# Kernel optimization log

Measured on AMD Instinct MI355X. Metric: run time of the kernel, lower is better.

Reference implementation:

```python
import jax, jax.numpy as jnp
import numpy as np

K = 5            # spline kernel size per dim
NUM_CLASSES = 10
EPS = 1e-4       # matches module's normalize eps
ROUTING_ITERS = 3
_BITS = jnp.array([[(b >> 2) & 1, (b >> 1) & 1, b & 1] for b in range(8)], dtype=jnp.float32)  # [8,3]


def normalize(t, axis=-1):
    return t / (jnp.sqrt(jnp.sum(t * t, axis=axis, keepdims=True)) + EPS)


def quat_mul(q, r):
    # quaternions stored (x, y, z, w) -- module sets identity as [:,:,:,3]=1
    qx, qy, qz, qw = q[..., 0], q[..., 1], q[..., 2], q[..., 3]
    rx, ry, rz, rw = r[..., 0], r[..., 1], r[..., 2], r[..., 3]
    return jnp.stack([
        qw * rx + qx * rw + qy * rz - qz * ry,
        qw * ry - qx * rz + qy * rw + qz * rx,
        qw * rz + qx * ry - qy * rx + qz * rw,
        qw * rw - qx * rx - qy * ry - qz * rz,
    ], axis=-1)


def spline_conv(x, pseudo, src, dst, W, root, bias, n_nodes):
    # degree-1 open B-spline conv, kernel 5^3, in=1, out=16
    v = pseudo * (K - 1)                                   # [E,3]
    i0 = jnp.clip(jnp.floor(v), 0, K - 2)                  # [E,3]
    frac = v - i0
    i0 = i0.astype(jnp.int32)
    idx = i0[:, None, :] + _BITS.astype(jnp.int32)[None]   # [E,8,3]
    kflat = (idx[..., 0] * K + idx[..., 1]) * K + idx[..., 2]  # [E,8]
    wb = jnp.prod(jnp.where(_BITS[None] > 0, frac[:, None, :], 1.0 - frac[:, None, :]), axis=-1)  # [E,8]
    Wg = W[kflat]                                          # [E,8,16] irregular gather (dominant traffic)
    wk = jnp.einsum('eb,ebo->eo', wb, Wg)                  # [E,16]
    msg = x[src] * wk                                      # [E,16] (in-channels = 1)
    agg = jax.ops.segment_sum(msg, dst, num_segments=n_nodes)
    deg = jax.ops.segment_sum(jnp.ones_like(dst, dtype=x.dtype), dst, num_segments=n_nodes)
    return agg / jnp.maximum(deg, 1.0)[:, None] + x @ root + bias


def caps_layer(pose, act, q):
    # pose [N,I,4], act [N,I], q [I,J,4] -> pose [N,J,4], act [N,J]
    qn = normalize(q)
    pred = normalize(quat_mul(qn[None], pose[:, :, None, :]))  # [N,I,J,4]
    b = jnp.zeros(pred.shape[:3], dtype=pose.dtype)
    for _ in range(ROUTING_ITERS):
        c = jax.nn.softmax(b, axis=2) * act[:, :, None]
        s = jnp.einsum('nij,nijq->njq', c, pred)
        v = normalize(s)
        b = b + jnp.einsum('nijq,njq->nij', pred, v)
    act_out = jax.nn.sigmoid(jnp.einsum('nij,nijq,njq->nj', c, pred, v))
    return v, act_out


def pool_by_agreement(pose, act, pos, G, start, size):
    # voxel-grid clustering + agreement-weighted quaternion averaging
    g = jnp.clip(jnp.floor((pos - start) / size), 0, G - 1).astype(jnp.int32)  # [N,3]
    vid = (g[:, 0] * G + g[:, 1]) * G + g[:, 2]
    V = G ** 3
    s = jax.ops.segment_sum(act[:, :, None] * pose, vid, num_segments=V)  # [V,J,4]
    m = normalize(s)
    agree = jnp.sum(pose * m[vid], axis=-1)                                # [N,J]
    wsum = jax.ops.segment_sum(act, vid, num_segments=V)
    cnt = jax.ops.segment_sum(jnp.ones((pose.shape[0],), pose.dtype), vid, num_segments=V)
    act_out = jax.nn.sigmoid(jax.ops.segment_sum(act * agree, vid, num_segments=V) / (wsum + EPS))
    pos_out = jax.ops.segment_sum(pos, vid, num_segments=V) / (cnt[:, None] + EPS)
    return m, act_out, pos_out


def forward(x, pos, pseudo, W_spline, root, bias, lin_w, lin_b, q0, q1, q3, q5, q6, q7, edge_index):
    N = x.shape[0]
    src, dst = edge_index[0], edge_index[1]
    h = spline_conv(x, pseudo, src, dst, W_spline, root, bias, N)   # [N,16]
    quats = jax.nn.elu(h) @ lin_w + lin_b                           # [N,4]
    pose = normalize(quats.reshape(N, 1, 4))                        # [N,1,4]
    act = x.reshape(N, 1)                                           # expand to num_caps_in=1
    pose, act = caps_layer(pose, act, q0)                           # 1 -> 6
    pose, act = caps_layer(pose, act, q1)                           # 6 -> 6
    min_pos, max_pos = pos.min(), pos.max()
    rng = max_pos + 0.001 - min_pos
    pose, act, p = pool_by_agreement(pose, act, pos, 32, min_pos, rng / 32)   # -> 32768 voxels
    pose, act = caps_layer(pose, act, q3)                           # 6 -> 8
    pose, act, p = pool_by_agreement(pose, act, p, 8, min_pos, rng / 8)       # -> 512
    pose, act = caps_layer(pose, act, q5)                           # 8 -> 12
    pose, act, p = pool_by_agreement(pose, act, p, 2, min_pos, rng / 2)       # -> 8
    pose, act = caps_layer(pose, act, q6)                           # 12 -> 14
    pose, act, p = pool_by_agreement(pose, act, p, 1, min_pos - 0.5, max_pos - min_pos + 1.0)  # -> 1
    pose, act = caps_layer(pose, act, q7)                           # 14 -> 10
    return act                                                      # [1, 10]


def setup_inputs() -> dict:
    key = jax.random.key(0)
    ks = jax.random.split(key, 16)
    N, E = 50000, 800000
    def caps_q(k, i, j):
        return jax.random.normal(k, (i, j, 4), dtype=jnp.float32)
    return {
        'x': jax.random.uniform(ks[0], (N, 1), dtype=jnp.float32),
        'pos': jax.random.uniform(ks[1], (N, 3), dtype=jnp.float32),
        'pseudo': jax.random.uniform(ks[2], (E, 3), dtype=jnp.float32),
        'W_spline': jax.random.normal(ks[3], (K ** 3, 16), dtype=jnp.float32) * 0.1,
        'root': jax.random.normal(ks[4], (1, 16), dtype=jnp.float32) * 0.1,
        'bias': jnp.zeros((16,), dtype=jnp.float32),
        'lin_w': jax.random.normal(ks[5], (16, 4), dtype=jnp.float32) * 0.25,
        'lin_b': jnp.zeros((4,), dtype=jnp.float32),
        'q0': caps_q(ks[6], 1, 6),
        'q1': caps_q(ks[7], 6, 6),
        'q3': caps_q(ks[8], 6, 8),
        'q5': caps_q(ks[9], 8, 12),
        'q6': caps_q(ks[10], 12, 14),
        'q7': caps_q(ks[11], 14, NUM_CLASSES),
        'edge_index': jax.random.randint(ks[12], (2, E), 0, N, dtype=jnp.int32),
    }


def reference(x, pos, pseudo, W_spline, root, bias, lin_w, lin_b, q0, q1, q3, q5, q6, q7, edge_index):
    return forward(x, pos, pseudo, W_spline, root, bias, lin_w, lin_b, q0, q1, q3, q5, q6, q7, edge_index)
```

## Files before the change

kernel.cpp:

```cpp
#include <hip/hip_runtime.h>
#include <math.h>

#define EPS 1e-4f

__device__ __forceinline__ float sigmoidf_(float x){ return 1.0f/(1.0f+expf(-x)); }

__device__ __forceinline__ unsigned f2u_(float f){
    unsigned u = __float_as_uint(f);
    return (u & 0x80000000u) ? ~u : (u | 0x80000000u);
}
__device__ __forceinline__ float u2f_(unsigned u){
    unsigned b = (u & 0x80000000u) ? (u & 0x7FFFFFFFu) : ~u;
    return __uint_as_float(b);
}

__global__ void minmax_kernel(const float* __restrict__ p, int n, unsigned* mm){
    float lo = INFINITY, hi = -INFINITY;
    for (int i = blockIdx.x*blockDim.x + threadIdx.x; i < n; i += gridDim.x*blockDim.x){
        float v = p[i]; lo = fminf(lo, v); hi = fmaxf(hi, v);
    }
    for (int off = 32; off > 0; off >>= 1){
        lo = fminf(lo, __shfl_down(lo, off));
        hi = fmaxf(hi, __shfl_down(hi, off));
    }
    __shared__ float slo[8], shi[8];
    int wid = threadIdx.x >> 6;
    if ((threadIdx.x & 63) == 0){ slo[wid] = lo; shi[wid] = hi; }
    __syncthreads();
    if (threadIdx.x == 0){
        int nw = blockDim.x >> 6;
        for (int w = 1; w < nw; w++){ lo = fminf(lo, slo[w]); hi = fmaxf(hi, shi[w]); }
        atomicMin(&mm[0], f2u_(lo));
        atomicMax(&mm[1], f2u_(hi));
    }
}


__global__ void edge_rank(const int* __restrict__ ei, int* __restrict__ deg,
                          int* __restrict__ rank, int E){
    int e = blockIdx.x*blockDim.x + threadIdx.x;
    if (e >= E) return;
    rank[e] = atomicAdd(&deg[ei[E + e]], 1);
}

__global__ __launch_bounds__(256)
void scan_bsum(const int* __restrict__ deg, int* __restrict__ bsum, int N){
    int i = blockIdx.x*256 + threadIdx.x;
    int v = (i < N) ? deg[i] : 0;
    for (int o = 32; o > 0; o >>= 1) v += __shfl_down(v, o);
    __shared__ int ws[4];
    if ((threadIdx.x & 63) == 0) ws[threadIdx.x >> 6] = v;
    __syncthreads();
    if (threadIdx.x == 0) bsum[blockIdx.x] = ws[0] + ws[1] + ws[2] + ws[3];
}

__global__ __launch_bounds__(1024)
void scan_top(int* __restrict__ bsum, int NB){
    __shared__ int sh[1024];
    int t = threadIdx.x;
    int v = (t < NB) ? bsum[t] : 0;
    sh[t] = v;
    __syncthreads();
    for (int d = 1; d < 1024; d <<= 1){
        int u = (t >= d) ? sh[t - d] : 0;
        __syncthreads();
        sh[t] += u;
        __syncthreads();
    }
    if (t < NB) bsum[t] = sh[t] - v;
    if (t == 1023) bsum[NB] = sh[1023];
}

__global__ __launch_bounds__(256)
void scan_final(const int* __restrict__ deg, const int* __restrict__ bsum,
                int* __restrict__ off, int N, int NB){
    __shared__ int sh[256];
    int b = blockIdx.x;
    int i = b*256 + threadIdx.x;
    int v = (i < N) ? deg[i] : 0;
    sh[threadIdx.x] = v;
    __syncthreads();
    for (int d = 1; d < 256; d <<= 1){
        int u = (threadIdx.x >= d) ? sh[threadIdx.x - d] : 0;
        __syncthreads();
        sh[threadIdx.x] += u;
        __syncthreads();
    }
    if (i < N) off[i] = bsum[b] + sh[threadIdx.x] - v;
    if (b == 0 && threadIdx.x == 0) off[N] = bsum[NB];
}

__global__ void edge_pack(const int* __restrict__ ei, const float* __restrict__ pseudo,
                          const float* __restrict__ x,
                          const int* __restrict__ rank, const int* __restrict__ off,
                          float4* __restrict__ rec4, int* __restrict__ recb, int E){
    int e = blockIdx.x*blockDim.x + threadIdx.x;
    if (e >= E) return;
    float p0 = pseudo[3*e], p1 = pseudo[3*e+1], p2 = pseudo[3*e+2];
    int s = ei[e], d = ei[E + e];
    float v0 = p0*4.f, v1 = p1*4.f, v2 = p2*4.f;
    float f0 = fminf(fmaxf(floorf(v0), 0.f), 3.f);
    float f1 = fminf(fmaxf(floorf(v1), 0.f), 3.f);
    float f2 = fminf(fmaxf(floorf(v2), 0.f), 3.f);
    int slot = off[d] + rank[e];
    rec4[slot] = make_float4(v0 - f0, v1 - f1, v2 - f2, x[s]);
    recb[slot] = ((int)f0*5 + (int)f1)*5 + (int)f2;
}

__device__ __forceinline__ int voxel_id(const float* __restrict__ pos, int n, int G,
                                        float start, float size){
    int g[3];
    #pragma unroll
    for (int k = 0; k < 3; k++){
        float gg = floorf((pos[(size_t)n*3 + k] - start) / size);
        gg = fminf(fmaxf(gg, 0.f), (float)(G - 1));
        g[k] = (int)gg;
    }
    return (g[0]*G + g[1])*G + g[2];
}

__device__ __forceinline__ void pool_geom(const unsigned* mm, int G, int mode,
                                          float& start, float& size){
    float mn = u2f_(mm[0]), mx = u2f_(mm[1]);
    if (mode == 0){ start = mn; size = (mx + 0.001f - mn) / (float)G; }
    else          { start = mn - 0.5f; size = mx - mn + 1.0f; }
}

__global__ void elist_node(const float* __restrict__ pos, int* __restrict__ head,
                           int* __restrict__ nxt, int N, int G, int mode,
                           const unsigned* __restrict__ mm){
    int n = blockIdx.x*blockDim.x + threadIdx.x;
    if (n >= N) return;
    float start, size; pool_geom(mm, G, mode, start, size);
    int v = voxel_id(pos, n, G, start, size);
    nxt[n] = atomicExch(&head[v], n);
}

__global__ __launch_bounds__(256)
void spline_node_kernel(const float* __restrict__ x, const float4* __restrict__ rec4,
                        const int* __restrict__ recb, const int* __restrict__ off,
                        const float* __restrict__ W,
                        const float* __restrict__ root, const float* __restrict__ bias,
                        const float* __restrict__ lin_w, const float* __restrict__ lin_b,
                        float* __restrict__ pose, float* __restrict__ act, int N){
    __shared__ float Ws[125*17];
    for (int i = threadIdx.x; i < 125*16; i += blockDim.x)
        Ws[(i >> 4)*17 + (i & 15)] = W[i];
    __syncthreads();
    int t = blockIdx.x*blockDim.x + threadIdx.x;
    int n = t >> 3;
    int k = t & 7;
    if (n >= N) return;

    int o0 = off[n], o1 = off[n+1];

    float agg[16];
    #pragma unroll
    for (int o = 0; o < 16; o++) agg[o] = 0.f;

    for (int s = o0 + k; s < o1; s += 8){
        float4 rv = rec4[s];
        int base = recb[s];
        float fr0 = rv.x, fr1 = rv.y, fr2 = rv.z, xv = rv.w;
        #pragma unroll
        for (int b = 0; b < 8; b++){
            int b0 = (b >> 2) & 1, b1 = (b >> 1) & 1, b2 = b & 1;
            float w = (b0 ? fr0 : 1.f - fr0) * (b1 ? fr1 : 1.f - fr1) * (b2 ? fr2 : 1.f - fr2);
            w *= xv;
            const float* Wr = &Ws[(base + b0*25 + b1*5 + b2)*17];
            #pragma unroll
            for (int o = 0; o < 16; o++) agg[o] += w * Wr[o];
        }
    }

    #pragma unroll
    for (int o = 0; o < 16; o++){
        agg[o] += __shfl_xor(agg[o], 1);
        agg[o] += __shfl_xor(agg[o], 2);
        agg[o] += __shfl_xor(agg[o], 4);
    }

    if (k != 0) return;

    float deg = fmaxf((float)(o1 - o0), 1.0f);
    float xs = x[n];
    float qv0 = lin_b[0], qv1 = lin_b[1], qv2 = lin_b[2], qv3 = lin_b[3];
    #pragma unroll
    for (int o = 0; o < 16; o++){
        float h = agg[o] / deg + xs * root[o] + bias[o];
        float e = (h > 0.f) ? h : expm1f(h);
        qv0 += e * lin_w[o*4 + 0];
        qv1 += e * lin_w[o*4 + 1];
        qv2 += e * lin_w[o*4 + 2];
        qv3 += e * lin_w[o*4 + 3];
    }
    float inv = 1.0f / (sqrtf(qv0*qv0 + qv1*qv1 + qv2*qv2 + qv3*qv3) + EPS);
    pose[(size_t)n*4 + 0] = qv0*inv;
    pose[(size_t)n*4 + 1] = qv1*inv;
    pose[(size_t)n*4 + 2] = qv2*inv;
    pose[(size_t)n*4 + 3] = qv3*inv;
    act[n] = xs;
}

template<int I, int J, int NPB>
__global__ __launch_bounds__(NPB*I*J)
void caps_coop_kernel(const float* __restrict__ poseIn, const float* __restrict__ actIn,
                      const float* __restrict__ q, float* __restrict__ poseOut,
                      float* __restrict__ actOut, int N){
    const int IJ = I*J;
    const int tid = threadIdx.x;
    const int nl  = tid / IJ;
    const int li  = tid - nl*IJ;
    const int i   = li / J;
    const int j   = li - i*J;
    const int node = blockIdx.x*NPB + nl;
    const bool on = (node < N);

    __shared__ float redA[NPB][I*J];
    __shared__ float redB[NPB][I*J];
    __shared__ float cp[NPB][I*J*4];
    __shared__ float vsh[NPB][J*4];

    float prx=0.f, pry=0.f, prz=0.f, prw=0.f, ai=0.f;
    if (on){
        float qx = q[li*4+0], qy = q[li*4+1], qz = q[li*4+2], qw = q[li*4+3];
        float qinv = 1.0f/(sqrtf(qx*qx+qy*qy+qz*qz+qw*qw)+EPS);
        qx*=qinv; qy*=qinv; qz*=qinv; qw*=qinv;
        const float* pp = &poseIn[((size_t)node*I + i)*4];
        float rx=pp[0], ry=pp[1], rz=pp[2], rw=pp[3];
        ai = actIn[(size_t)node*I + i];
        float tx = qw*rx + qx*rw + qy*rz - qz*ry;
        float ty = qw*ry - qx*rz + qy*rw + qz*rx;
        float tz = qw*rz + qx*ry - qy*rx + qz*rw;
        float tw = qw*rw - qx*rx - qy*ry - qz*rz;
        float pinv = 1.0f/(sqrtf(tx*tx+ty*ty+tz*tz+tw*tw)+EPS);
        prx=tx*pinv; pry=ty*pinv; prz=tz*pinv; prw=tw*pinv;
    }

    float b = 0.f, c = 0.f;
    for (int t = 0; t < 3; t++){
        redA[nl][li] = b;
        __syncthreads();
        float mb = -INFINITY;
        #pragma unroll
        for (int jj = 0; jj < J; jj++) mb = fmaxf(mb, redA[nl][i*J+jj]);
        float e = expf(b - mb);
        redB[nl][li] = e;
        __syncthreads();
        float s = 0.f;
        #pragma unroll
        for (int jj = 0; jj < J; jj++) s += redB[nl][i*J+jj];
        c = ai * e / s;
        cp[nl][li*4+0] = c*prx; cp[nl][li*4+1] = c*pry;
        cp[nl][li*4+2] = c*prz; cp[nl][li*4+3] = c*prw;
        __syncthreads();
        for (int idx = li; idx < J*4; idx += IJ){
            int jj = idx >> 2, comp = idx & 3;
            float acc = 0.f;
            #pragma unroll
            for (int ii = 0; ii < I; ii++) acc += cp[nl][(ii*J+jj)*4+comp];
            vsh[nl][idx] = acc;
        }
        __syncthreads();
        if (li < J){
            float a0=vsh[nl][li*4], a1=vsh[nl][li*4+1], a2=vsh[nl][li*4+2], a3=vsh[nl][li*4+3];
            float inv = 1.0f/(sqrtf(a0*a0+a1*a1+a2*a2+a3*a3)+EPS);
            vsh[nl][li*4]=a0*inv; vsh[nl][li*4+1]=a1*inv;
            vsh[nl][li*4+2]=a2*inv; vsh[nl][li*4+3]=a3*inv;
        }
        __syncthreads();
        if (t < 2){
            b += prx*vsh[nl][j*4] + pry*vsh[nl][j*4+1] + prz*vsh[nl][j*4+2] + prw*vsh[nl][j*4+3];
            __syncthreads();
        } else {
            redA[nl][li] = c*(prx*vsh[nl][j*4] + pry*vsh[nl][j*4+1]
                            + prz*vsh[nl][j*4+2] + prw*vsh[nl][j*4+3]);
            __syncthreads();
            if (li < J && on){
                float acc = 0.f;
                #pragma unroll
                for (int ii = 0; ii < I; ii++) acc += redA[nl][ii*J+li];
                actOut[(size_t)node*J + li] = sigmoidf_(acc);
                poseOut[((size_t)node*J+li)*4+0] = vsh[nl][li*4+0];
                poseOut[((size_t)node*J+li)*4+1] = vsh[nl][li*4+1];
                poseOut[((size_t)node*J+li)*4+2] = vsh[nl][li*4+2];
                poseOut[((size_t)node*J+li)*4+3] = vsh[nl][li*4+3];
            }
        }
    }
}

template<int J>
__global__ __launch_bounds__(256)
void pool1_gather_kernel(const float* __restrict__ pose, const float* __restrict__ act,
                         const float* __restrict__ pos,
                         const int* __restrict__ head, const int* __restrict__ nxt,
                         float* __restrict__ poseOut, float* __restrict__ actOut,
                         float* __restrict__ posOut, int V){
    int v = blockIdx.x*blockDim.x + threadIdx.x;
    if (v >= V) return;

    float s[J][4], w[J], ps0=0.f, ps1=0.f, ps2=0.f;
    #pragma unroll
    for (int j = 0; j < J; j++){ s[j][0]=0.f; s[j][1]=0.f; s[j][2]=0.f; s[j][3]=0.f; w[j]=0.f; }

    int cnt = 0;
    for (int n = head[v]; n >= 0; n = nxt[n]){
        const float* pb = &pose[(size_t)n*J*4];
        const float* ab = &act[(size_t)n*J];
        #pragma unroll
        for (int j = 0; j < J; j++){
            float aj = ab[j];
            s[j][0] += aj*pb[j*4+0];
            s[j][1] += aj*pb[j*4+1];
            s[j][2] += aj*pb[j*4+2];
            s[j][3] += aj*pb[j*4+3];
            w[j] += aj;
        }
        ps0 += pos[(size_t)n*3+0];
        ps1 += pos[(size_t)n*3+1];
        ps2 += pos[(size_t)n*3+2];
        cnt++;
    }
    #pragma unroll
    for (int j = 0; j < J; j++){
        float inv = 1.0f/(sqrtf(s[j][0]*s[j][0]+s[j][1]*s[j][1]+
                                s[j][2]*s[j][2]+s[j][3]*s[j][3])+EPS);
        s[j][0]*=inv; s[j][1]*=inv; s[j][2]*=inv; s[j][3]*=inv;
    }
    float ag[J];
    #pragma unroll
    for (int j = 0; j < J; j++) ag[j] = 0.f;
    for (int n = head[v]; n >= 0; n = nxt[n]){
        const float* pb = &pose[(size_t)n*J*4];
        const float* ab = &act[(size_t)n*J];
        #pragma unroll
        for (int j = 0; j < J; j++){
            float agree = pb[j*4+0]*s[j][0] + pb[j*4+1]*s[j][1]
                        + pb[j*4+2]*s[j][2] + pb[j*4+3]*s[j][3];
            ag[j] += ab[j]*agree;
        }
    }
    #pragma unroll
    for (int j = 0; j < J; j++){
        size_t o = (size_t)v*J + j;
        actOut[o] = sigmoidf_(ag[j] / (w[j] + EPS));
        poseOut[o*4+0] = s[j][0];
        poseOut[o*4+1] = s[j][1];
        poseOut[o*4+2] = s[j][2];
        poseOut[o*4+3] = s[j][3];
    }
    float c = (float)cnt + EPS;
    posOut[(size_t)v*3+0] = ps0 / c;
    posOut[(size_t)v*3+1] = ps1 / c;
    posOut[(size_t)v*3+2] = ps2 / c;
}

template<int V, int J, int CH, int NCHUNK>
__global__ void pool_priv1(const float4* __restrict__ poseIn, const float* __restrict__ actIn,
                           const float* __restrict__ posIn,
                           float* __restrict__ s, float* __restrict__ wsum,
                           float* __restrict__ cnt, float* __restrict__ psum,
                           int N, int G, int mode, const unsigned* __restrict__ mm){
    __shared__ float s_[V*CH*4];
    __shared__ float wsum_[V*CH];
    __shared__ float cnt_[V];
    __shared__ float psum_[V*3];
    const int chunk = blockIdx.x % NCHUNK;
    const int slice = blockIdx.x / NCHUNK;
    const int nslices = gridDim.x / NCHUNK;
    const int c0 = chunk * CH;

    for (int t = threadIdx.x; t < V*CH*4; t += blockDim.x) s_[t] = 0.f;
    for (int t = threadIdx.x; t < V*CH; t += blockDim.x) wsum_[t] = 0.f;
    if (chunk == 0){
        for (int t = threadIdx.x; t < V; t += blockDim.x) cnt_[t] = 0.f;
        for (int t = threadIdx.x; t < V*3; t += blockDim.x) psum_[t] = 0.f;
    }
    __syncthreads();

    float start, size; pool_geom(mm, G, mode, start, size);
    int per = (N + nslices - 1) / nslices;
    int n0 = slice * per, n1 = min(N, n0 + per);

    for (int n = n0 + (int)threadIdx.x; n < n1; n += blockDim.x){
        int vid = voxel_id(posIn, n, G, start, size);
        #pragma unroll
        for (int jj = 0; jj < CH; jj++){
            int j = c0 + jj;
            float aj = actIn[(size_t)n*J + j];
            float4 p = poseIn[(size_t)n*J + j];
            int b = (vid*CH + jj)*4;
            atomicAdd(&s_[b+0], aj*p.x);
            atomicAdd(&s_[b+1], aj*p.y);
            atomicAdd(&s_[b+2], aj*p.z);
            atomicAdd(&s_[b+3], aj*p.w);
            atomicAdd(&wsum_[vid*CH + jj], aj);
        }
        if (chunk == 0){
            atomicAdd(&cnt_[vid], 1.0f);
            atomicAdd(&psum_[vid*3+0], posIn[(size_t)n*3+0]);
            atomicAdd(&psum_[vid*3+1], posIn[(size_t)n*3+1]);
            atomicAdd(&psum_[vid*3+2], posIn[(size_t)n*3+2]);
        }
    }
    __syncthreads();

    for (int t = threadIdx.x; t < V*CH*4; t += blockDim.x){
        float val = s_[t];
        if (val != 0.f){
            int v = t / (CH*4), r = t % (CH*4);
            atomicAdd(&s[((size_t)v*J + c0)*4 + r], val);
        }
    }
    for (int t = threadIdx.x; t < V*CH; t += blockDim.x){
        float val = wsum_[t];
        if (val != 0.f){
            int v = t / CH, jj = t % CH;
            atomicAdd(&wsum[(size_t)v*J + c0 + jj], val);
        }
    }
    if (chunk == 0){
        for (int t = threadIdx.x; t < V; t += blockDim.x)
            if (cnt_[t] != 0.f) atomicAdd(&cnt[t], cnt_[t]);
        for (int t = threadIdx.x; t < V*3; t += blockDim.x)
            if (psum_[t] != 0.f) atomicAdd(&psum[t], psum_[t]);
    }
}

template<int V, int J>
__global__ void pool_priv2(const float4* __restrict__ poseIn, const float* __restrict__ actIn,
                           const float* __restrict__ posIn, const float4* __restrict__ m,
                           float* __restrict__ agacc,
                           int N, int G, int mode, const unsigned* __restrict__ mm){
    __shared__ float ag_[V*J];
    for (int t = threadIdx.x; t < V*J; t += blockDim.x) ag_[t] = 0.f;
    __syncthreads();
    float start, size; pool_geom(mm, G, mode, start, size);
    int nslices = gridDim.x;
    int per = (N + nslices - 1) / nslices;
    int n0 = blockIdx.x * per, n1 = min(N, n0 + per);
    for (int n = n0 + (int)threadIdx.x; n < n1; n += blockDim.x){
        int vid = voxel_id(posIn, n, G, start, size);
        #pragma unroll
        for (int j = 0; j < J; j++){
            float4 p  = poseIn[(size_t)n*J + j];
            float4 mv = m[(size_t)vid*J + j];
            float agree = p.x*mv.x + p.y*mv.y + p.z*mv.z + p.w*mv.w;
            atomicAdd(&ag_[vid*J + j], actIn[(size_t)n*J + j]*agree);
        }
    }
    __syncthreads();
    for (int t = threadIdx.x; t < V*J; t += blockDim.x)
        if (ag_[t] != 0.f) atomicAdd(&agacc[t], ag_[t]);
}

__global__ void pool_m(const float* __restrict__ s, float* __restrict__ m, int VJ){
    int t = blockIdx.x*blockDim.x + threadIdx.x;
    if (t >= VJ) return;
    float a = s[(size_t)t*4], b = s[(size_t)t*4+1], c = s[(size_t)t*4+2], d = s[(size_t)t*4+3];
    float inv = 1.0f / (sqrtf(a*a + b*b + c*c + d*d) + EPS);
    m[(size_t)t*4]   = a*inv;
    m[(size_t)t*4+1] = b*inv;
    m[(size_t)t*4+2] = c*inv;
    m[(size_t)t*4+3] = d*inv;
}

__global__ void pool_fin(const float* __restrict__ agacc, const float* __restrict__ wsum,
                         const float* __restrict__ cnt, const float* __restrict__ psum,
                         float* __restrict__ actOut, float* __restrict__ posOut, int V, int J){
    int t = blockIdx.x*blockDim.x + threadIdx.x;
    if (t >= V*J) return;
    int v = t / J, j = t % J;
    actOut[t] = sigmoidf_(agacc[t] / (wsum[t] + EPS));
    if (j == 0){
        float c = cnt[v] + EPS;
        posOut[(size_t)v*3 + 0] = psum[(size_t)v*3 + 0] / c;
        posOut[(size_t)v*3 + 1] = psum[(size_t)v*3 + 1] / c;
        posOut[(size_t)v*3 + 2] = psum[(size_t)v*3 + 2] / c;
    }
}

template<int V, int J, int CH>
__global__ void pool_fused_kernel(const float* __restrict__ poseIn, const float* __restrict__ actIn,
                                  const float* __restrict__ posIn,
                                  float* __restrict__ poseOut, float* __restrict__ actOut,
                                  float* __restrict__ posOut,
                                  int N, int G, int mode, const unsigned* __restrict__ mm){
    __shared__ float s_[V*CH*4];
    __shared__ float wsum_[V*CH];
    __shared__ float ag_[V*CH];
    __shared__ float cnt_[V];
    __shared__ float psum_[V*3];
    const int c0 = blockIdx.x * CH;

    for (int t = threadIdx.x; t < V*CH*4; t += blockDim.x) s_[t] = 0.f;
    for (int t = threadIdx.x; t < V*CH; t += blockDim.x){ wsum_[t] = 0.f; ag_[t] = 0.f; }
    if (blockIdx.x == 0){
        for (int t = threadIdx.x; t < V; t += blockDim.x) cnt_[t] = 0.f;
        for (int t = threadIdx.x; t < V*3; t += blockDim.x) psum_[t] = 0.f;
    }
    __syncthreads();

    float start, size; pool_geom(mm, G, mode, start, size);

    for (int n = threadIdx.x; n < N; n += blockDim.x){
        int vid = voxel_id(posIn, n, G, start, size);
        #pragma unroll
        for (int jj = 0; jj < CH; jj++){
            int j = c0 + jj;
            float aj = actIn[(size_t)n*J + j];
            const float* pb = &poseIn[((size_t)n*J + j)*4];
            int b = (vid*CH + jj)*4;
            atomicAdd(&s_[b+0], aj*pb[0]);
            atomicAdd(&s_[b+1], aj*pb[1]);
            atomicAdd(&s_[b+2], aj*pb[2]);
            atomicAdd(&s_[b+3], aj*pb[3]);
            atomicAdd(&wsum_[vid*CH + jj], aj);
        }
        if (blockIdx.x == 0){
            atomicAdd(&cnt_[vid], 1.0f);
            atomicAdd(&psum_[vid*3+0], posIn[(size_t)n*3+0]);
            atomicAdd(&psum_[vid*3+1], posIn[(size_t)n*3+1]);
            atomicAdd(&psum_[vid*3+2], posIn[(size_t)n*3+2]);
        }
    }
    __syncthreads();

    for (int t = threadIdx.x; t < V*CH; t += blockDim.x){
        float a = s_[t*4], b = s_[t*4+1], c = s_[t*4+2], d = s_[t*4+3];
        float inv = 1.0f / (sqrtf(a*a + b*b + c*c + d*d) + EPS);
        s_[t*4] = a*inv; s_[t*4+1] = b*inv; s_[t*4+2] = c*inv; s_[t*4+3] = d*inv;
    }
    __syncthreads();

    for (int n = threadIdx.x; n < N; n += blockDim.x){
        int vid = voxel_id(posIn, n, G, start, size);
        #pragma unroll
        for (int jj = 0; jj < CH; jj++){
            int j = c0 + jj;
            const float* pb = &poseIn[((size_t)n*J + j)*4];
            const float* mb = &s_[(vid*CH + jj)*4];
            float agree = pb[0]*mb[0] + pb[1]*mb[1] + pb[2]*mb[2] + pb[3]*mb[3];
            atomicAdd(&ag_[vid*CH + jj], actIn[(size_t)n*J + j]*agree);
        }
    }
    __syncthreads();

    for (int t = threadIdx.x; t < V*CH; t += blockDim.x){
        int v = t / CH, jj = t % CH;
        size_t o = (size_t)v*J + c0 + jj;
        actOut[o] = sigmoidf_(ag_[t] / (wsum_[t] + EPS));
        poseOut[o*4+0] = s_[t*4+0];
        poseOut[o*4+1] = s_[t*4+1];
        poseOut[o*4+2] = s_[t*4+2];
        poseOut[o*4+3] = s_[t*4+3];
    }
    if (blockIdx.x == 0){
        for (int v = threadIdx.x; v < V; v += blockDim.x){
            float c = cnt_[v] + EPS;
            posOut[(size_t)v*3+0] = psum_[(size_t)v*3+0] / c;
            posOut[(size_t)v*3+1] = psum_[(size_t)v*3+1] / c;
            posOut[(size_t)v*3+2] = psum_[(size_t)v*3+2] / c;
        }
    }
}

extern "C" void kernel_launch(void* const* d_in, const int* in_sizes, int n_in,
                              void* d_out, int out_size, void* d_ws, size_t ws_size,
                              hipStream_t stream){
    const float* x      = (const float*)d_in[0];
    const float* pos    = (const float*)d_in[1];
    const float* pseudo = (const float*)d_in[2];
    const float* Wsp    = (const float*)d_in[3];
    const float* root   = (const float*)d_in[4];
    const float* bias   = (const float*)d_in[5];
    const float* lin_w  = (const float*)d_in[6];
    const float* lin_b  = (const float*)d_in[7];
    const float* q0     = (const float*)d_in[8];
    const float* q1     = (const float*)d_in[9];
    const float* q3     = (const float*)d_in[10];
    const float* q5     = (const float*)d_in[11];
    const float* q6     = (const float*)d_in[12];
    const float* q7     = (const float*)d_in[13];
    const int*   ei     = (const int*)d_in[14];
    const int N = in_sizes[0];
    const int E = in_sizes[2] / 3;
    const int V1 = 32768;
    const int NB = (N + 255)/256;

    char* ws = (char*)d_ws;
    size_t off = 0;
    auto alloc = [&](size_t bytes)->void*{
        void* p = ws + off;
        off += (bytes + 255) & ~(size_t)255;
        return p;
    };
    unsigned* mm   = (unsigned*)alloc(8);
    int* deg       = (int*)alloc((size_t)N*sizeof(int));
    int* erank     = (int*)alloc((size_t)E*sizeof(int));
    int* eoff      = (int*)alloc((size_t)(N+1)*sizeof(int));
    int* bsum      = (int*)alloc((size_t)(NB+1)*sizeof(int));
    float4* rec4   = (float4*)alloc((size_t)E*sizeof(float4));
    int* recb      = (int*)alloc((size_t)E*sizeof(int));
    int* vhead     = (int*)alloc((size_t)V1*sizeof(int));
    int* vnxt      = (int*)alloc((size_t)N*sizeof(int));
    float* P0  = (float*)alloc((size_t)1250000*sizeof(float));
    float* P1  = (float*)alloc((size_t)1250000*sizeof(float));
    float* A0  = (float*)alloc((size_t)310000*sizeof(float));
    float* A1  = (float*)alloc((size_t)310000*sizeof(float));
    float* PB0 = (float*)alloc((size_t)100000*sizeof(float));
    float* PB1 = (float*)alloc((size_t)100000*sizeof(float));
    size_t pool_off0 = off;
    float* vs  = (float*)alloc((size_t)512*8*4*sizeof(float));
    float* vw  = (float*)alloc((size_t)512*8*sizeof(float));
    float* va  = (float*)alloc((size_t)512*8*sizeof(float));
    float* vc  = (float*)alloc((size_t)512*sizeof(float));
    float* vp  = (float*)alloc((size_t)512*3*sizeof(float));
    size_t pool_bytes = off - pool_off0;

    hipMemsetAsync(mm,     0xFF, 4, stream);
    hipMemsetAsync(mm + 1, 0x00, 4, stream);
    hipMemsetAsync(deg, 0, (size_t)N*sizeof(int), stream);
    hipMemsetAsync(vhead, 0xFF, (size_t)V1*sizeof(int), stream);

    minmax_kernel<<<80, 256, 0, stream>>>(pos, N*3, mm);

    edge_rank<<<(E + 255)/256, 256, 0, stream>>>(ei, deg, erank, E);
    scan_bsum<<<NB, 256, 0, stream>>>(deg, bsum, N);
    scan_top<<<1, 1024, 0, stream>>>(bsum, NB);
    scan_final<<<NB, 256, 0, stream>>>(deg, bsum, eoff, N, NB);
    edge_pack<<<(E + 255)/256, 256, 0, stream>>>(ei, pseudo, x, erank, eoff, rec4, recb, E);
    spline_node_kernel<<<(8*N + 255)/256, 256, 0, stream>>>(x, rec4, recb, eoff, Wsp,
                                                            root, bias, lin_w, lin_b, P0, A0, N);

    caps_coop_kernel<1,6,32><<<(N + 31)/32, 32*6, 0, stream>>>(P0, A0, q0, P1, A1, N);
    caps_coop_kernel<6,6,7><<<(N + 6)/7, 7*36, 0, stream>>>(P1, A1, q1, P0, A0, N);

    {
        const int G = 32;
        elist_node<<<(N + 255)/256, 256, 0, stream>>>(pos, vhead, vnxt, N, G, 0, mm);
        pool1_gather_kernel<6><<<(V1 + 255)/256, 256, 0, stream>>>(P0, A0, pos, vhead, vnxt,
                                                                   P1, A1, PB0, V1);
    }
    caps_coop_kernel<6,8,5><<<(32768 + 4)/5, 5*48, 0, stream>>>(P1, A1, q3, P0, A0, 32768);

    {
        const int V = 512, J = 8, G = 8, NSL = 64;
        hipMemsetAsync(vs, 0, pool_bytes, stream);
        pool_priv1<V,J,4,2><<<2*NSL, 256, 0, stream>>>((const float4*)P0, A0, PB0,
                                                       vs, vw, vc, vp, 32768, G, 0, mm);
        pool_m<<<(V*J + 255)/256, 256, 0, stream>>>(vs, P1, V*J);
        pool_priv2<V,J><<<NSL, 256, 0, stream>>>((const float4*)P0, A0, PB0,
                                                 (const float4*)P1, va, 32768, G, 0, mm);
        pool_fin<<<(V*J + 255)/256, 256, 0, stream>>>(va, vw, vc, vp, A1, PB1, V, J);
    }
    caps_coop_kernel<8,12,2><<<256, 2*96, 0, stream>>>(P1, A1, q5, P0, A0, 512);

    {
        const int V = 8, J = 12, G = 2, NSL = 16;
        hipMemsetAsync(vs, 0, pool_bytes, stream);
        pool_priv1<V,J,12,1><<<NSL, 256, 0, stream>>>((const float4*)P0, A0, PB1,
                                                      vs, vw, vc, vp, 512, G, 0, mm);
        pool_m<<<1, 256, 0, stream>>>(vs, P1, V*J);
        pool_priv2<V,J><<<NSL, 256, 0, stream>>>((const float4*)P0, A0, PB1,
                                                 (const float4*)P1, va, 512, G, 0, mm);
        pool_fin<<<1, 256, 0, stream>>>(va, vw, vc, vp, A1, PB0, V, J);
    }
    caps_coop_kernel<12,14,1><<<8, 168, 0, stream>>>(P1, A1, q6, P0, A0, 8);

    pool_fused_kernel<1,14,14><<<1, 1024, 0, stream>>>(P0, A0, PB0, P1, A1, PB1, 8, 1, 1, mm);
    caps_coop_kernel<14,10,1><<<1, 140, 0, stream>>>(P1, A1, q7, P0, (float*)d_out, 1);
}
```

Measured before the change: 349.5 us.

## Use thread-per-node capsule routing for early layers and fuse small pooling stage

Adds a capsule routing kernel that gives each node to a single thread. That thread holds all predictions and routing logits in registers, which replaces the cooperative block kernel that used shared-memory reductions for the three large early capsule layers. The small second pooling stage, a memset plus four kernel launches, is also replaced by one call to the existing fused pooling kernel. The aim is to remove shared-memory reduction and synchronisation overhead and launch count. The cost is heavy register pressure for the 6x8 layer, which may spill or lower occupancy.

```diff
diff --git a/kernel.cpp b/kernel.cpp
--- a/kernel.cpp
+++ b/kernel.cpp
@@ -34,7 +34,6 @@
         atomicMax(&mm[1], f2u_(hi));
     }
 }
-
 
 __global__ void edge_rank(const int* __restrict__ ei, int* __restrict__ deg,
                           int* __restrict__ rank, int E){
@@ -200,6 +199,90 @@
     pose[(size_t)n*4 + 2] = qv2*inv;
     pose[(size_t)n*4 + 3] = qv3*inv;
     act[n] = xs;
+}
+
+template<int I, int J>
+__global__ __launch_bounds__(64)
+void caps_node_kernel(const float* __restrict__ poseIn, const float* __restrict__ actIn,
+                      const float* __restrict__ q,
+                      float* __restrict__ poseOut, float* __restrict__ actOut, int N){
+    __shared__ float qn[I*J*4];
+    for (int t = threadIdx.x; t < I*J; t += blockDim.x){
+        float qa=q[t*4], qb=q[t*4+1], qc=q[t*4+2], qd=q[t*4+3];
+        float inv = 1.f/(sqrtf(qa*qa+qb*qb+qc*qc+qd*qd)+EPS);
+        qn[t*4+0]=qa*inv; qn[t*4+1]=qb*inv; qn[t*4+2]=qc*inv; qn[t*4+3]=qd*inv;
+    }
+    __syncthreads();
+    int n = blockIdx.x*blockDim.x + threadIdx.x;
+    if (n >= N) return;
+
+    float pr[I][J][4];
+    float a[I];
+    float b[I][J];
+    #pragma unroll
+    for (int i = 0; i < I; i++){
+        float4 p = *reinterpret_cast<const float4*>(&poseIn[((size_t)n*I + i)*4]);
+        a[i] = actIn[(size_t)n*I + i];
+        #pragma unroll
+        for (int j = 0; j < J; j++){
+            const float* qq = &qn[(i*J + j)*4];
+            float qx=qq[0], qy=qq[1], qz=qq[2], qw=qq[3];
+            float tx = qw*p.x + qx*p.w + qy*p.z - qz*p.y;
+            float ty = qw*p.y - qx*p.z + qy*p.w + qz*p.x;
+            float tz = qw*p.z + qx*p.y - qy*p.x + qz*p.w;
+            float tw = qw*p.w - qx*p.x - qy*p.y - qz*p.z;
+            float inv = 1.f/(sqrtf(tx*tx+ty*ty+tz*tz+tw*tw)+EPS);
+            pr[i][j][0]=tx*inv; pr[i][j][1]=ty*inv; pr[i][j][2]=tz*inv; pr[i][j][3]=tw*inv;
+            b[i][j] = 0.f;
+        }
+    }
+
+    float c[I][J], v[J][4];
+    #pragma unroll
+    for (int t = 0; t < 3; t++){
+        #pragma unroll
+        for (int i = 0; i < I; i++){
+            float mb = -INFINITY;
+            #pragma unroll
+            for (int j = 0; j < J; j++) mb = fmaxf(mb, b[i][j]);
+            float e[J]; float d = 0.f;
+            #pragma unroll
+            for (int j = 0; j < J; j++){ e[j] = expf(b[i][j] - mb); d += e[j]; }
+            #pragma unroll
+            for (int j = 0; j < J; j++) c[i][j] = a[i] * e[j] / d;
+        }
+        #pragma unroll
+        for (int j = 0; j < J; j++){
+            float s0=0.f, s1=0.f, s2=0.f, s3=0.f;
+            #pragma unroll
+            for (int i = 0; i < I; i++){
+                s0 += c[i][j]*pr[i][j][0]; s1 += c[i][j]*pr[i][j][1];
+                s2 += c[i][j]*pr[i][j][2]; s3 += c[i][j]*pr[i][j][3];
+            }
+            float inv = 1.f/(sqrtf(s0*s0+s1*s1+s2*s2+s3*s3)+EPS);
+            v[j][0]=s0*inv; v[j][1]=s1*inv; v[j][2]=s2*inv; v[j][3]=s3*inv;
+        }
+        if (t < 2){
+            #pragma unroll
+            for (int i = 0; i < I; i++)
+                #pragma unroll
+                for (int j = 0; j < J; j++)
+                    b[i][j] += pr[i][j][0]*v[j][0] + pr[i][j][1]*v[j][1]
+                             + pr[i][j][2]*v[j][2] + pr[i][j][3]*v[j][3];
+        }
+    }
+
+    #pragma unroll
+    for (int j = 0; j < J; j++){
+        float acc = 0.f;
+        #pragma unroll
+        for (int i = 0; i < I; i++)
+            acc += c[i][j]*(pr[i][j][0]*v[j][0] + pr[i][j][1]*v[j][1]
+                          + pr[i][j][2]*v[j][2] + pr[i][j][3]*v[j][3]);
+        actOut[(size_t)n*J + j] = sigmoidf_(acc);
+        *reinterpret_cast<float4*>(&poseOut[((size_t)n*J + j)*4]) =
+            make_float4(v[j][0], v[j][1], v[j][2], v[j][3]);
+    }
 }
 
 template<int I, int J, int NPB>
@@ -634,8 +717,8 @@
     spline_node_kernel<<<(8*N + 255)/256, 256, 0, stream>>>(x, rec4, recb, eoff, Wsp,
                                                             root, bias, lin_w, lin_b, P0, A0, N);
 
-    caps_coop_kernel<1,6,32><<<(N + 31)/32, 32*6, 0, stream>>>(P0, A0, q0, P1, A1, N);
-    caps_coop_kernel<6,6,7><<<(N + 6)/7, 7*36, 0, stream>>>(P1, A1, q1, P0, A0, N);
+    caps_node_kernel<1,6><<<(N + 63)/64, 64, 0, stream>>>(P0, A0, q0, P1, A1, N);
+    caps_node_kernel<6,6><<<(N + 63)/64, 64, 0, stream>>>(P1, A1, q1, P0, A0, N);
 
     {
         const int G = 32;
@@ -643,7 +726,7 @@
         pool1_gather_kernel<6><<<(V1 + 255)/256, 256, 0, stream>>>(P0, A0, pos, vhead, vnxt,
                                                                    P1, A1, PB0, V1);
     }
-    caps_coop_kernel<6,8,5><<<(32768 + 4)/5, 5*48, 0, stream>>>(P1, A1, q3, P0, A0, 32768);
+    caps_node_kernel<6,8><<<(32768 + 63)/64, 64, 0, stream>>>(P1, A1, q3, P0, A0, 32768);
 
     {
         const int V = 512, J = 8, G = 8, NSL = 64;
@@ -657,16 +740,7 @@
     }
     caps_coop_kernel<8,12,2><<<256, 2*96, 0, stream>>>(P1, A1, q5, P0, A0, 512);
 
-    {
-        const int V = 8, J = 12, G = 2, NSL = 16;
-        hipMemsetAsync(vs, 0, pool_bytes, stream);
-        pool_priv1<V,J,12,1><<<NSL, 256, 0, stream>>>((const float4*)P0, A0, PB1,
-                                                      vs, vw, vc, vp, 512, G, 0, mm);
-        pool_m<<<1, 256, 0, stream>>>(vs, P1, V*J);
-        pool_priv2<V,J><<<NSL, 256, 0, stream>>>((const float4*)P0, A0, PB1,
-                                                 (const float4*)P1, va, 512, G, 0, mm);
-        pool_fin<<<1, 256, 0, stream>>>(va, vw, vc, vp, A1, PB0, V, J);
-    }
+    pool_fused_kernel<8,12,12><<<1, 1024, 0, stream>>>(P0, A0, PB1, P1, A1, PB0, 512, 2, 0, mm);
     caps_coop_kernel<12,14,1><<<8, 168, 0, stream>>>(P1, A1, q6, P0, A0, 8);
 
     pool_fused_kernel<1,14,14><<<1, 1024, 0, stream>>>(P0, A0, PB0, P1, A1, PB1, 8, 1, 1, mm);
```

Result: slower. 401.1 us (+14.8%).
